# Kernel optimization log

Measured on AMD Instinct MI355X. Metric: run time of the kernel, lower is better.

Reference implementation:

```python
import jax, jax.numpy as jnp
import numpy as np

B, NQ, S, D = 2, 2048, 2048, 1024
H, HD, OUT = 16, 64, 1024


def setup_inputs() -> dict:
    key = jax.random.key(0)
    ks = jax.random.split(key, 8)
    scale = 1.0 / np.sqrt(D)
    return {
        "queries": jax.random.normal(ks[0], (B, NQ, D), jnp.float32),
        "keys": jax.random.normal(ks[1], (B, S, D), jnp.float32),
        "values": jax.random.normal(ks[2], (B, S, D), jnp.float32),
        "indicators": jax.random.uniform(ks[3], (B, S), jnp.float32),
        "Wq": jax.random.normal(ks[4], (D, H * HD), jnp.float32) * scale,
        "Wk": jax.random.normal(ks[5], (D, H * HD), jnp.float32) * scale,
        "Wv": jax.random.normal(ks[6], (D, H * HD), jnp.float32) * scale,
        "Wo": jax.random.normal(ks[7], (H * HD, OUT), jnp.float32) * scale,
    }


def reference(queries, keys, values, indicators, Wq, Wk, Wv, Wo):
    b, nq, _ = queries.shape
    s = keys.shape[1]
    # projections -> [b, len, H, HD] -> [b, H, len, HD]
    Q = (queries @ Wq).reshape(b, nq, H, HD).transpose(0, 2, 1, 3)
    K = (keys @ Wk).reshape(b, s, H, HD).transpose(0, 2, 1, 3)
    V = (values @ Wv).reshape(b, s, H, HD).transpose(0, 2, 1, 3)
    # scores [b, H, nq, s], softmax over s, THEN multiplicative mask
    scores = jnp.einsum("bhqd,bhkd->bhqk", Q, K) / jnp.sqrt(jnp.float32(HD))
    probs = jax.nn.softmax(scores, axis=-1)
    probs = probs * indicators[:, None, None, :]  # post-softmax mask
    ctx = jnp.einsum("bhqk,bhkd->bhqd", probs, V)
    ctx = ctx.transpose(0, 2, 1, 3).reshape(b, nq, H * HD)
    return ctx @ Wo
```

## Files before the change

kernel.cpp:

```cpp
#include <hip/hip_runtime.h>


typedef float f32x4 __attribute__((ext_vector_type(4)));
typedef __bf16 bf16x8 __attribute__((ext_vector_type(8)));
typedef __bf16 bf16x4 __attribute__((ext_vector_type(4)));

#define DEVINL __device__ __forceinline__

DEVINL void gll16(const void* g, void* l) {
  __builtin_amdgcn_global_load_lds((const __attribute__((address_space(1))) void*)g,
                                   (__attribute__((address_space(3))) void*)l, 16, 0, 0);
}
DEVINL bf16x8 ldfrag(const void* p) { return __builtin_bit_cast(bf16x8, *(const int4*)p); }
DEVINL f32x4 mfma16(bf16x8 a, bf16x8 b, f32x4 c) {
  return __builtin_amdgcn_mfma_f32_16x16x32_bf16(a, b, c, 0, 0, 0);
}

__global__ void cvt_qkv(const float* __restrict__ q, const float* __restrict__ k,
                        const float* __restrict__ v, __bf16* __restrict__ qo,
                        __bf16* __restrict__ ko, __bf16* __restrict__ vo) {
  const float* s = blockIdx.y == 0 ? q : (blockIdx.y == 1 ? k : v);
  __bf16* d = blockIdx.y == 0 ? qo : (blockIdx.y == 1 ? ko : vo);
  size_t i = ((size_t)blockIdx.x * blockDim.x + threadIdx.x) * 4;
  float4 f = *(const float4*)(s + i);
  bf16x4 o = {(__bf16)f.x, (__bf16)f.y, (__bf16)f.z, (__bf16)f.w};
  *(bf16x4*)(d + i) = o;
}

__global__ void wtrans(const float* __restrict__ Wq, const float* __restrict__ Wk,
                       const float* __restrict__ Wv, const float* __restrict__ Wo,
                       __bf16* __restrict__ o0, __bf16* __restrict__ o1,
                       __bf16* __restrict__ o2, __bf16* __restrict__ o3) {
  __shared__ float tl[32][33];
  int z = blockIdx.z;
  const float* W = z == 0 ? Wq : z == 1 ? Wk : z == 2 ? Wv : Wo;
  __bf16* o = z == 0 ? o0 : z == 1 ? o1 : z == 2 ? o2 : o3;
  float scale = z == 0 ? 0.125f * 1.44269504f : 1.0f;
  int c0 = blockIdx.x * 32, r0 = blockIdx.y * 32;
  int tx = threadIdx.x, ty = threadIdx.y;
#pragma unroll
  for (int rr = 0; rr < 32; rr += 8)
    tl[rr + ty][tx] = W[(size_t)(r0 + rr + ty) * 1024 + c0 + tx];
  __syncthreads();
#pragma unroll
  for (int cc = 0; cc < 32; cc += 8)
    o[(size_t)(c0 + cc + ty) * 1024 + r0 + tx] = (__bf16)(tl[tx][cc + ty] * scale);
}

template <int MT>
DEVINL void gemm_core(const __bf16* __restrict__ A, const __bf16* __restrict__ Bt,
                      int K, int m0, int n0, char* As, char* Bs, f32x4 (&acc)[MT][4],
                      int t) {
  const int lane = t & 63, wv = t >> 6;
  const int li = lane & 15, g = lane >> 4;
  const int wr = wv >> 1, wc = wv & 1;
  const size_t lda = (size_t)K * 2;
  for (int kt = 0; kt < K; kt += 32) {
    if (kt) __syncthreads();
#pragma unroll
    for (int p = 0; p < MT / 2; ++p) {
      int off = p * 4096 + t * 16;
      int row = off >> 6, ch = (off >> 4) & 3;
      int gch = ch ^ ((row >> 1) & 3);
      gll16((const char*)A + (size_t)(m0 + row) * lda + (size_t)kt * 2 + gch * 16,
            As + off);
    }
#pragma unroll
    for (int p = 0; p < 2; ++p) {
      int off = p * 4096 + t * 16;
      int row = off >> 6, ch = (off >> 4) & 3;
      int gch = ch ^ ((row >> 1) & 3);
      gll16((const char*)Bt + (size_t)(n0 + row) * lda + (size_t)kt * 2 + gch * 16,
            Bs + off);
    }
    __syncthreads();
    bf16x8 af[MT], bfr[4];
#pragma unroll
    for (int mt = 0; mt < MT; ++mt) {
      int row = wr * (MT * 16) + mt * 16 + li;
      int gch = g ^ ((row >> 1) & 3);
      af[mt] = ldfrag(As + row * 64 + gch * 16);
    }
#pragma unroll
    for (int nt = 0; nt < 4; ++nt) {
      int row = wc * 64 + nt * 16 + li;
      int gch = g ^ ((row >> 1) & 3);
      bfr[nt] = ldfrag(Bs + row * 64 + gch * 16);
    }
#pragma unroll
    for (int mt = 0; mt < MT; ++mt)
#pragma unroll
      for (int nt = 0; nt < 4; ++nt)
        acc[mt][nt] = mfma16(af[mt], bfr[nt], acc[mt][nt]);
  }
}

__global__ __launch_bounds__(256) void gemm_qkv(
    const __bf16* __restrict__ qb, const __bf16* __restrict__ kb,
    const __bf16* __restrict__ vb, const __bf16* __restrict__ WqT,
    const __bf16* __restrict__ WkT, const __bf16* __restrict__ WvT,
    const float* __restrict__ ind, __bf16* __restrict__ Qp, __bf16* __restrict__ Kp,
    __bf16* __restrict__ Vtp) {
  __shared__ __align__(16) char As[4 * 2048];
  __shared__ __align__(16) char Bs[8192];
  const int z = blockIdx.z;
  const __bf16* A = z == 0 ? qb : z == 1 ? kb : vb;
  const __bf16* Bt = z == 0 ? WqT : z == 1 ? WkT : WvT;
  const int m0 = blockIdx.y * 128, n0 = blockIdx.x * 128;
  f32x4 acc[4][4] = {};
  gemm_core<4>(A, Bt, 1024, m0, n0, As, Bs, acc, threadIdx.x);
  const int lane = threadIdx.x & 63, wv = threadIdx.x >> 6;
  const int li = lane & 15, g = lane >> 4;
  const int wr = wv >> 1, wc = wv & 1;
#pragma unroll
  for (int mt = 0; mt < 4; ++mt)
#pragma unroll
    for (int nt = 0; nt < 4; ++nt) {
      int m = m0 + wr * 64 + mt * 16 + g * 4;
      int n = n0 + wc * 64 + nt * 16 + li;
      if (z < 2) {
        __bf16* Cb = z ? Kp : Qp;
#pragma unroll
        for (int r = 0; r < 4; ++r)
          Cb[(size_t)(m + r) * 1024 + n] = (__bf16)acc[mt][nt][r];
      } else {
        float4 i4 = *(const float4*)(ind + m);
        bf16x4 o = {(__bf16)(acc[mt][nt][0] * i4.x), (__bf16)(acc[mt][nt][1] * i4.y),
                    (__bf16)(acc[mt][nt][2] * i4.z), (__bf16)(acc[mt][nt][3] * i4.w)};
        *(bf16x4*)(Vtp + (size_t)n * 4096 + m) = o;
      }
    }
}

__global__ __launch_bounds__(256) void gemm_out(const __bf16* __restrict__ ctx,
                                                const __bf16* __restrict__ WoT,
                                                float* __restrict__ out) {
  __shared__ __align__(16) char As[2 * 2048];
  __shared__ __align__(16) char Bs[8192];
  const int m0 = blockIdx.y * 64, n0 = blockIdx.x * 128;
  f32x4 acc[2][4] = {};
  gemm_core<2>(ctx, WoT, 1024, m0, n0, As, Bs, acc, threadIdx.x);
  const int lane = threadIdx.x & 63, wv = threadIdx.x >> 6;
  const int li = lane & 15, g = lane >> 4;
  const int wr = wv >> 1, wc = wv & 1;
#pragma unroll
  for (int mt = 0; mt < 2; ++mt)
#pragma unroll
    for (int nt = 0; nt < 4; ++nt) {
      int m = m0 + wr * 32 + mt * 16 + g * 4;
      int n = n0 + wc * 64 + nt * 16 + li;
#pragma unroll
      for (int r = 0; r < 4; ++r) out[(size_t)(m + r) * 1024 + n] = acc[mt][nt][r];
    }
}

__global__ __launch_bounds__(256) void flash_k(const __bf16* __restrict__ Qp,
                                               const __bf16* __restrict__ Kp,
                                               const __bf16* __restrict__ Vt,
                                               __bf16* __restrict__ ctx) {
  __shared__ __align__(16) char smem[35840];
  char* kv = smem;
  char* qps = smem + 16384;
  const int t = threadIdx.x;
  const int lane = t & 63, wv = t >> 6;
  const int li = lane & 15, g = lane >> 4;
  const int qt = blockIdx.x & 15, h = (blockIdx.x >> 4) & 15, b = blockIdx.x >> 8;
  const size_t qrow0 = (size_t)b * 2048 + (size_t)qt * 128;
  char* psw = qps + wv * 4864;

#pragma unroll
  for (int p = 0; p < 4; ++p) {
    int off = p * 4096 + t * 16;
    int row = off >> 7, ch = (off >> 4) & 7;
    int gch = ch ^ (row & 7);
    gll16((const char*)Qp + ((qrow0 + row) * 1024 + h * 64) * 2 + gch * 16, qps + off);
  }
  __syncthreads();

  bf16x8 qf[2][2];
#pragma unroll
  for (int nt = 0; nt < 2; ++nt)
#pragma unroll
    for (int ks = 0; ks < 2; ++ks) {
      int row = wv * 32 + nt * 16 + li;
      int gch = (4 * ks + g) ^ (row & 7);
      qf[nt][ks] = ldfrag(qps + row * 128 + gch * 16);
    }

  f32x4 acc[4][2] = {};
  float lsum[2] = {0.0f, 0.0f};

  for (int kt = 0; kt < 32; ++kt) {
    __syncthreads();
#pragma unroll
    for (int p = 0; p < 2; ++p) {
      int off = p * 4096 + t * 16;
      int row = off >> 7, ch = (off >> 4) & 7;
      int gch = ch ^ (row & 7);
      gll16((const char*)Kp +
                (((size_t)b * 2048 + kt * 64 + row) * 1024 + h * 64) * 2 + gch * 16,
            kv + off);
      gll16((const char*)Vt +
                ((size_t)(h * 64 + row) * 4096 + (size_t)b * 2048 + kt * 64) * 2 +
                gch * 16,
            kv + 8192 + off);
    }
    __syncthreads();

    f32x4 st[4][2] = {};
#pragma unroll
    for (int ks = 0; ks < 2; ++ks)
#pragma unroll
      for (int mt = 0; mt < 4; ++mt) {
        int row = mt * 16 + li;
        int gch = (4 * ks + g) ^ (row & 7);
        bf16x8 kf = ldfrag(kv + row * 128 + gch * 16);
        st[mt][0] = mfma16(kf, qf[0][ks], st[mt][0]);
        st[mt][1] = mfma16(kf, qf[1][ks], st[mt][1]);
      }

#pragma unroll
    for (int nt = 0; nt < 2; ++nt) {
      float rs = 0.0f;
#pragma unroll
      for (int mt = 0; mt < 4; ++mt) {
        float p0 = __builtin_amdgcn_exp2f(st[mt][nt][0]);
        float p1 = __builtin_amdgcn_exp2f(st[mt][nt][1]);
        float p2 = __builtin_amdgcn_exp2f(st[mt][nt][2]);
        float p3 = __builtin_amdgcn_exp2f(st[mt][nt][3]);
        rs += (p0 + p1) + (p2 + p3);
        bf16x4 pv = {(__bf16)p0, (__bf16)p1, (__bf16)p2, (__bf16)p3};
        *(bf16x4*)(psw + (nt * 16 + li) * 152 + mt * 32 + g * 8) = pv;
      }
      lsum[nt] += rs;
    }

#pragma unroll
    for (int kc = 0; kc < 2; ++kc) {
      bf16x8 pf0 = ldfrag(psw + li * 152 + kc * 64 + g * 16);
      bf16x8 pf1 = ldfrag(psw + (16 + li) * 152 + kc * 64 + g * 16);
#pragma unroll
      for (int mtd = 0; mtd < 4; ++mtd) {
        int row = mtd * 16 + li;
        int gch = (4 * kc + g) ^ (row & 7);
        bf16x8 vf = ldfrag(kv + 8192 + row * 128 + gch * 16);
        acc[mtd][0] = mfma16(vf, pf0, acc[mtd][0]);
        acc[mtd][1] = mfma16(vf, pf1, acc[mtd][1]);
      }
    }
  }

#pragma unroll
  for (int nt = 0; nt < 2; ++nt) {
    float l = lsum[nt];
    l += __shfl_xor(l, 16);
    l += __shfl_xor(l, 32);
    float linv = 1.0f / l;
    size_t qrow = qrow0 + wv * 32 + nt * 16 + li;
#pragma unroll
    for (int mtd = 0; mtd < 4; ++mtd) {
      bf16x4 o = {(__bf16)(acc[mtd][nt][0] * linv), (__bf16)(acc[mtd][nt][1] * linv),
                  (__bf16)(acc[mtd][nt][2] * linv), (__bf16)(acc[mtd][nt][3] * linv)};
      *(bf16x4*)(ctx + qrow * 1024 + h * 64 + mtd * 16 + g * 4) = o;
    }
  }
}

extern "C" void kernel_launch(void* const* d_in, const int* in_sizes, int n_in,
                              void* d_out, int out_size, void* d_ws, size_t ws_size,
                              hipStream_t stream) {
  const float* q = (const float*)d_in[0];
  const float* k = (const float*)d_in[1];
  const float* v = (const float*)d_in[2];
  const float* ind = (const float*)d_in[3];
  const float* Wq = (const float*)d_in[4];
  const float* Wk = (const float*)d_in[5];
  const float* Wv = (const float*)d_in[6];
  const float* Wo = (const float*)d_in[7];
  char* ws = (char*)d_ws;
  const size_t MB = 1024 * 1024;
  __bf16* qb = (__bf16*)(ws + 0);
  __bf16* kb = (__bf16*)(ws + 8 * MB);
  __bf16* vb = (__bf16*)(ws + 16 * MB);
  __bf16* WqT = (__bf16*)(ws + 24 * MB);
  __bf16* WkT = (__bf16*)(ws + 26 * MB);
  __bf16* WvT = (__bf16*)(ws + 28 * MB);
  __bf16* WoT = (__bf16*)(ws + 30 * MB);
  __bf16* Qp = (__bf16*)(ws + 32 * MB);
  __bf16* Kp = (__bf16*)(ws + 40 * MB);
  __bf16* Vtp = (__bf16*)(ws + 48 * MB);
  __bf16* ctx = (__bf16*)(ws + 0);
  float* out = (float*)d_out;

  cvt_qkv<<<dim3(4096, 3), 256, 0, stream>>>(q, k, v, qb, kb, vb);
  wtrans<<<dim3(32, 32, 4), dim3(32, 8), 0, stream>>>(Wq, Wk, Wv, Wo, WqT, WkT, WvT,
                                                      WoT);
  gemm_qkv<<<dim3(8, 32, 3), 256, 0, stream>>>(qb, kb, vb, WqT, WkT, WvT, ind, Qp, Kp,
                                               Vtp);
  flash_k<<<dim3(512), 256, 0, stream>>>(Qp, Kp, Vtp, ctx);
  gemm_out<<<dim3(8, 64), 256, 0, stream>>>(ctx, WoT, out);
}
```

Before: 247.8 us.

## Split flash attention over KV halves with combine kernel; merge prep kernels

The attention kernel now splits the key sequence into two halves, launching twice as many blocks. Each block writes a partial normalized context plus its row-sum, and a new combine kernel merges the two halves weighted by those sums. This is meant to raise occupancy on the many-CU GPU, since 512 blocks underfill it. It costs extra global traffic for the partial outputs and one more launch. The bf16 conversion and weight transpose kernels are also fused into a single launch to save launch overhead. The merge needs no max correction because the softmax has no running max, and the masking is folded into V upstream.

```diff
diff --git a/kernel.cpp b/kernel.cpp
--- a/kernel.cpp
+++ b/kernel.cpp
@@ -16,35 +16,40 @@
   return __builtin_amdgcn_mfma_f32_16x16x32_bf16(a, b, c, 0, 0, 0);
 }
 
-__global__ void cvt_qkv(const float* __restrict__ q, const float* __restrict__ k,
-                        const float* __restrict__ v, __bf16* __restrict__ qo,
-                        __bf16* __restrict__ ko, __bf16* __restrict__ vo) {
-  const float* s = blockIdx.y == 0 ? q : (blockIdx.y == 1 ? k : v);
-  __bf16* d = blockIdx.y == 0 ? qo : (blockIdx.y == 1 ? ko : vo);
-  size_t i = ((size_t)blockIdx.x * blockDim.x + threadIdx.x) * 4;
-  float4 f = *(const float4*)(s + i);
-  bf16x4 o = {(__bf16)f.x, (__bf16)f.y, (__bf16)f.z, (__bf16)f.w};
-  *(bf16x4*)(d + i) = o;
-}
-
-__global__ void wtrans(const float* __restrict__ Wq, const float* __restrict__ Wk,
-                       const float* __restrict__ Wv, const float* __restrict__ Wo,
-                       __bf16* __restrict__ o0, __bf16* __restrict__ o1,
-                       __bf16* __restrict__ o2, __bf16* __restrict__ o3) {
-  __shared__ float tl[32][33];
-  int z = blockIdx.z;
-  const float* W = z == 0 ? Wq : z == 1 ? Wk : z == 2 ? Wv : Wo;
-  __bf16* o = z == 0 ? o0 : z == 1 ? o1 : z == 2 ? o2 : o3;
-  float scale = z == 0 ? 0.125f * 1.44269504f : 1.0f;
-  int c0 = blockIdx.x * 32, r0 = blockIdx.y * 32;
-  int tx = threadIdx.x, ty = threadIdx.y;
-#pragma unroll
-  for (int rr = 0; rr < 32; rr += 8)
-    tl[rr + ty][tx] = W[(size_t)(r0 + rr + ty) * 1024 + c0 + tx];
-  __syncthreads();
-#pragma unroll
-  for (int cc = 0; cc < 32; cc += 8)
-    o[(size_t)(c0 + cc + ty) * 1024 + r0 + tx] = (__bf16)(tl[tx][cc + ty] * scale);
+__global__ __launch_bounds__(256) void prep_k(
+    const float* __restrict__ q, const float* __restrict__ k,
+    const float* __restrict__ v, const float* __restrict__ Wq,
+    const float* __restrict__ Wk, const float* __restrict__ Wv,
+    const float* __restrict__ Wo, __bf16* __restrict__ qo, __bf16* __restrict__ ko,
+    __bf16* __restrict__ vo, __bf16* __restrict__ o0, __bf16* __restrict__ o1,
+    __bf16* __restrict__ o2, __bf16* __restrict__ o3) {
+  const int bid = blockIdx.x;
+  const int t = threadIdx.x;
+  if (bid < 12288) {
+    int plane = bid >> 12, bx = bid & 4095;
+    const float* s = plane == 0 ? q : (plane == 1 ? k : v);
+    __bf16* d = plane == 0 ? qo : (plane == 1 ? ko : vo);
+    size_t i = ((size_t)bx * 256 + t) * 4;
+    float4 f = *(const float4*)(s + i);
+    bf16x4 o = {(__bf16)f.x, (__bf16)f.y, (__bf16)f.z, (__bf16)f.w};
+    *(bf16x4*)(d + i) = o;
+  } else {
+    __shared__ float tl[32][33];
+    int wid = bid - 12288;
+    int z = wid >> 10, x = wid & 31, y = (wid >> 5) & 31;
+    const float* W = z == 0 ? Wq : z == 1 ? Wk : z == 2 ? Wv : Wo;
+    __bf16* o = z == 0 ? o0 : z == 1 ? o1 : z == 2 ? o2 : o3;
+    float scale = z == 0 ? 0.125f * 1.44269504f : 1.0f;
+    int c0 = x * 32, r0 = y * 32;
+    int tx = t & 31, ty = t >> 5;
+#pragma unroll
+    for (int rr = 0; rr < 32; rr += 8)
+      tl[rr + ty][tx] = W[(size_t)(r0 + rr + ty) * 1024 + c0 + tx];
+    __syncthreads();
+#pragma unroll
+    for (int cc = 0; cc < 32; cc += 8)
+      o[(size_t)(c0 + cc + ty) * 1024 + r0 + tx] = (__bf16)(tl[tx][cc + ty] * scale);
+  }
 }
 
 template <int MT>
@@ -157,15 +162,19 @@
 __global__ __launch_bounds__(256) void flash_k(const __bf16* __restrict__ Qp,
                                                const __bf16* __restrict__ Kp,
                                                const __bf16* __restrict__ Vt,
-                                               __bf16* __restrict__ ctx) {
+                                               __bf16* __restrict__ ctx0,
+                                               __bf16* __restrict__ ctx1,
+                                               float* __restrict__ pl) {
   __shared__ __align__(16) char smem[35840];
   char* kv = smem;
   char* qps = smem + 16384;
   const int t = threadIdx.x;
   const int lane = t & 63, wv = t >> 6;
   const int li = lane & 15, g = lane >> 4;
-  const int qt = blockIdx.x & 15, h = (blockIdx.x >> 4) & 15, b = blockIdx.x >> 8;
+  const int sp = blockIdx.x >> 9, rest = blockIdx.x & 511;
+  const int qt = rest & 15, h = (rest >> 4) & 15, b = rest >> 8;
   const size_t qrow0 = (size_t)b * 2048 + (size_t)qt * 128;
+  __bf16* ctx = sp ? ctx1 : ctx0;
   char* psw = qps + wv * 4864;
 
 #pragma unroll
@@ -190,7 +199,7 @@
   f32x4 acc[4][2] = {};
   float lsum[2] = {0.0f, 0.0f};
 
-  for (int kt = 0; kt < 32; ++kt) {
+  for (int kt = sp * 16; kt < sp * 16 + 16; ++kt) {
     __syncthreads();
 #pragma unroll
     for (int p = 0; p < 2; ++p) {
@@ -257,6 +266,7 @@
     l += __shfl_xor(l, 32);
     float linv = 1.0f / l;
     size_t qrow = qrow0 + wv * 32 + nt * 16 + li;
+    if (g == 0) pl[((size_t)sp * 4096 + qrow) * 16 + h] = l;
 #pragma unroll
     for (int mtd = 0; mtd < 4; ++mtd) {
       bf16x4 o = {(__bf16)(acc[mtd][nt][0] * linv), (__bf16)(acc[mtd][nt][1] * linv),
@@ -264,6 +274,24 @@
       *(bf16x4*)(ctx + qrow * 1024 + h * 64 + mtd * 16 + g * 4) = o;
     }
   }
+}
+
+__global__ __launch_bounds__(256) void combine_k(const __bf16* __restrict__ c0,
+                                                 const __bf16* __restrict__ c1,
+                                                 const float* __restrict__ pl,
+                                                 __bf16* __restrict__ ctx) {
+  size_t e = ((size_t)blockIdx.x * 256 + threadIdx.x) * 8;
+  int qrow = (int)(e >> 10), h = ((int)e & 1023) >> 6;
+  float l0 = pl[(size_t)qrow * 16 + h];
+  float l1 = pl[(size_t)(4096 + qrow) * 16 + h];
+  float w = 1.0f / (l0 + l1);
+  float w0 = l0 * w, w1 = l1 * w;
+  bf16x8 a = *(const bf16x8*)(c0 + e);
+  bf16x8 b = *(const bf16x8*)(c1 + e);
+  bf16x8 o;
+#pragma unroll
+  for (int i = 0; i < 8; ++i) o[i] = (__bf16)((float)a[i] * w0 + (float)b[i] * w1);
+  *(bf16x8*)(ctx + e) = o;
 }
 
 extern "C" void kernel_launch(void* const* d_in, const int* in_sizes, int n_in,
@@ -289,14 +317,17 @@
   __bf16* Qp = (__bf16*)(ws + 32 * MB);
   __bf16* Kp = (__bf16*)(ws + 40 * MB);
   __bf16* Vtp = (__bf16*)(ws + 48 * MB);
-  __bf16* ctx = (__bf16*)(ws + 0);
+  __bf16* ctx0 = (__bf16*)(ws + 0);
+  __bf16* ctx1 = (__bf16*)(ws + 8 * MB);
+  __bf16* ctx = (__bf16*)(ws + 16 * MB);
+  float* pl = (float*)(ws + 24 * MB);
   float* out = (float*)d_out;
 
-  cvt_qkv<<<dim3(4096, 3), 256, 0, stream>>>(q, k, v, qb, kb, vb);
-  wtrans<<<dim3(32, 32, 4), dim3(32, 8), 0, stream>>>(Wq, Wk, Wv, Wo, WqT, WkT, WvT,
-                                                      WoT);
+  prep_k<<<dim3(16384), 256, 0, stream>>>(q, k, v, Wq, Wk, Wv, Wo, qb, kb, vb, WqT,
+                                          WkT, WvT, WoT);
   gemm_qkv<<<dim3(8, 32, 3), 256, 0, stream>>>(qb, kb, vb, WqT, WkT, WvT, ind, Qp, Kp,
                                                Vtp);
-  flash_k<<<dim3(512), 256, 0, stream>>>(Qp, Kp, Vtp, ctx);
+  flash_k<<<dim3(1024), 256, 0, stream>>>(Qp, Kp, Vtp, ctx0, ctx1, pl);
+  combine_k<<<dim3(2048), 256, 0, stream>>>(ctx0, ctx1, pl, ctx);
   gemm_out<<<dim3(8, 64), 256, 0, stream>>>(ctx, WoT, out);
 }
```

Result: faster. 238.4 us (-3.8%).
